# Kernel tuning notes

Hardware: AMD Instinct MI355X
Metric: run time of the kernel (lower is better)

## Reference

```python
import jax, jax.numpy as jnp
import numpy as np

DIM = 256
N_EMBED = 1024
COMMITMENT_COST = 0.25


def setup_inputs() -> dict:
    key = jax.random.key(0)
    k1, k2 = jax.random.split(key)
    z = jax.random.normal(k1, (16, 256, 64, 64), dtype=jnp.float32)
    # nn.Embedding weight initialized uniform(-1/n_embed, 1/n_embed)
    embed = jax.random.uniform(k2, (N_EMBED, DIM), dtype=jnp.float32,
                               minval=-1.0 / N_EMBED, maxval=1.0 / N_EMBED)
    return {"z": z, "embed": embed}


def reference(z, embed):
    sg = jax.lax.stop_gradient
    # NCHW -> NHWC, flatten spatial+batch to tokens
    zp = jnp.transpose(z, (0, 2, 3, 1))            # [B,H,W,C]
    zf = zp.reshape(-1, DIM)                        # [N, C]
    # squared euclidean distances via expansion: |z|^2 + |e|^2 - 2 z.e
    d = (jnp.sum(zf * zf, axis=1, keepdims=True)
         + jnp.sum(embed * embed, axis=1)
         - 2.0 * zf @ embed.T)                      # [N, K]
    idx = jnp.argmin(d, axis=1)                     # [N]
    min_encodings = jax.nn.one_hot(idx, N_EMBED, dtype=zf.dtype)  # [N, K]
    # direct gather == one-hot @ embed (same math, one HBM pass)
    z_q = embed[idx].reshape(zp.shape)              # [B,H,W,C]
    loss = (jnp.mean((sg(z_q) - zp) ** 2)
            + COMMITMENT_COST * jnp.mean((z_q - sg(zp)) ** 2))
    # straight-through estimator
    z_q_st = zp + sg(z_q - zp)
    e_mean = jnp.mean(min_encodings, axis=0)
    perplexity = jnp.exp(-jnp.sum(e_mean * jnp.log(e_mean + 1e-10)))
    z_q_out = jnp.transpose(z_q_st, (0, 3, 1, 2))   # back to NCHW
    return (loss, z_q_out, perplexity, min_encodings, idx[:, None])
```

## Files before the change

### kernel.cpp

```cpp
#include <hip/hip_runtime.h>
#include <math.h>

#define DIM    256
#define K_EMB  1024
#define HW     4096
#define CHW    1048576
#define N_TOK  65536
#define NELEM  16777216

#define OUT_LOSS 0
#define OUT_ZQ   1
#define OUT_PERP 16777217
#define OUT_MENC 16777218LL
#define OUT_IDX  83886082

#define TAU  1.5e-4f

#define TAIL_ROW0  65216
#define FLAGS_OFF  66781184LL
#define FBS_OFF    66846720LL
#define EH_OFF     66912258LL

typedef short short8  __attribute__((ext_vector_type(8)));
typedef float floatx4 __attribute__((ext_vector_type(4)));
typedef float floatx2 __attribute__((ext_vector_type(2)));

__device__ __forceinline__ unsigned short f2bf(float f) {
    unsigned int u = __float_as_uint(f);
    return (unsigned short)((u + 0x7FFFu + ((u >> 16) & 1u)) >> 16);
}
__device__ __forceinline__ float bf2f(unsigned short h) {
    return __uint_as_float(((unsigned int)h) << 16);
}

__device__ __forceinline__ float np_pair128(const float* p) {
    float r[8];
    #pragma unroll
    for (int j = 0; j < 8; ++j) r[j] = p[j];
    for (int i = 8; i < 128; i += 8)
        #pragma unroll
        for (int j = 0; j < 8; ++j) r[j] = __fadd_rn(r[j], p[i + j]);
    return __fadd_rn(__fadd_rn(__fadd_rn(r[0], r[1]), __fadd_rn(r[2], r[3])),
                     __fadd_rn(__fadd_rn(r[4], r[5]), __fadd_rn(r[6], r[7])));
}
__device__ __forceinline__ float np_pair256(const float* p) {
    return __fadd_rn(np_pair128(p), np_pair128(p + 128));
}

__device__ __forceinline__ void build_frags(const float* __restrict__ zp, int quad, short8* a) {
    #pragma unroll
    for (int kc = 0; kc < 8; ++kc) {
        short8 vh, vl;
        #pragma unroll
        for (int u = 0; u < 8; ++u) {
            float v = __builtin_nontemporal_load(zp + (size_t)(kc * 32 + quad * 8 + u) * HW);
            unsigned short h = f2bf(v);
            vh[u] = (short)h;
            vl[u] = (short)f2bf(v - bf2f(h));
        }
        a[kc]     = vh;
        a[8 + kc] = vl;
    }
}

__global__ void t2_np_kernel(const float* __restrict__ embed, float* __restrict__ t2,
                             unsigned short* __restrict__ Eh) {
    int k = blockIdx.x * 256 + threadIdx.x;
    if (k >= K_EMB) return;
    const float* e = embed + (size_t)k * DIM;
    float p[256];
    for (int c = 0; c < DIM; c += 4) {
        float4 v = *(const float4*)(e + c);
        p[c]     = __fmul_rn(v.x, v.x);
        p[c + 1] = __fmul_rn(v.y, v.y);
        p[c + 2] = __fmul_rn(v.z, v.z);
        p[c + 3] = __fmul_rn(v.w, v.w);
    }
    t2[k] = np_pair256(p);
    unsigned short* dst = Eh + (size_t)k * DIM;
    for (int c0 = 0; c0 < DIM; c0 += 8) {
        short8 vh;
        #pragma unroll
        for (int u = 0; u < 8; ++u) vh[u] = (short)f2bf(e[c0 + u]);
        *(short8*)(dst + c0) = vh;
    }
}

__launch_bounds__(256, 4)
__global__ void vq_mfma(const float* __restrict__ z,
                        const unsigned short* __restrict__ Eh,
                        const float* __restrict__ t2g,
                        float* __restrict__ out,
                        unsigned int* __restrict__ nflag,
                        int* __restrict__ flags,
                        float* __restrict__ fbs) {
    __shared__ unsigned short lds_b[32 * 264];
    __shared__ float t2_lds[K_EMB];
    __shared__ int midx[64];

    const int tid  = threadIdx.x;
    const int lane = tid & 63;
    const int wv   = tid >> 6;
    const int l15  = lane & 15;
    const int quad = lane >> 4;
    const int m0   = blockIdx.x * 64;

    for (int i = tid; i < K_EMB; i += 256) t2_lds[i] = t2g[i];

    short8 a[16];
    {
        const int n = m0 + wv * 16 + l15;
        build_frags(z + (size_t)(n >> 12) * CHW + (n & 4095), quad, a);
    }

    float bs[4], ss[4]; int bk[4];
    #pragma unroll
    for (int r = 0; r < 4; ++r) { bs[r] = 3.4e38f; ss[r] = 3.4e38f; bk[r] = 0; }

    const int srow = tid >> 3;
    const int scol = (tid & 7) * 32;

    for (int it = 0; it < 32; ++it) {
        const int n0 = it * 32;
        __syncthreads();
        {
            const short8* g = (const short8*)(Eh + (size_t)(n0 + srow) * 256 + scol);
            short8* l = (short8*)(lds_b + srow * 264 + scol);
            short8 v0 = g[0], v1 = g[1], v2 = g[2], v3 = g[3];
            l[0] = v0; l[1] = v1; l[2] = v2; l[3] = v3;
        }
        __syncthreads();
        floatx4 acc0 = {0.f, 0.f, 0.f, 0.f};
        floatx4 acc1 = {0.f, 0.f, 0.f, 0.f};
        #pragma unroll
        for (int kc = 0; kc < 8; ++kc) {
            short8 b0 = *(const short8*)(lds_b + l15 * 264 + kc * 32 + quad * 8);
            short8 b1 = *(const short8*)(lds_b + (16 + l15) * 264 + kc * 32 + quad * 8);
            acc0 = __builtin_amdgcn_mfma_f32_16x16x32_bf16(a[kc],     b0, acc0, 0, 0, 0);
            acc1 = __builtin_amdgcn_mfma_f32_16x16x32_bf16(a[kc],     b1, acc1, 0, 0, 0);
            acc0 = __builtin_amdgcn_mfma_f32_16x16x32_bf16(a[8 + kc], b0, acc0, 0, 0, 0);
            acc1 = __builtin_amdgcn_mfma_f32_16x16x32_bf16(a[8 + kc], b1, acc1, 0, 0, 0);
        }
        float t20 = t2_lds[n0 + l15];
        float t21 = t2_lds[n0 + 16 + l15];
        #pragma unroll
        for (int r = 0; r < 4; ++r) {
            float s0 = fmaf(-2.0f, acc0[r], t20);
            if (s0 < bs[r]) { ss[r] = bs[r]; bs[r] = s0; bk[r] = n0 + l15; }
            else if (s0 < ss[r]) ss[r] = s0;
            float s1 = fmaf(-2.0f, acc1[r], t21);
            if (s1 < bs[r]) { ss[r] = bs[r]; bs[r] = s1; bk[r] = n0 + 16 + l15; }
            else if (s1 < ss[r]) ss[r] = s1;
        }
    }

    #pragma unroll
    for (int r = 0; r < 4; ++r) {
        for (int mo = 1; mo < 16; mo <<= 1) {
            float obs = __shfl_xor(bs[r], mo, 64);
            float oss = __shfl_xor(ss[r], mo, 64);
            int   obk = __shfl_xor(bk[r], mo, 64);
            if (obs < bs[r] || (obs == bs[r] && obk < bk[r])) {
                ss[r] = fminf(bs[r], oss); bs[r] = obs; bk[r] = obk;
            } else {
                ss[r] = fminf(ss[r], obs);
            }
        }
        if (l15 == 0) {
            int tl = wv * 16 + quad * 4 + r;
            out[OUT_IDX + m0 + tl] = (float)bk[r];
            midx[tl] = bk[r];
            if (ss[r] - bs[r] < TAU) {
                unsigned int slot = atomicAdd(nflag, 1u);
                flags[slot] = m0 + tl;
                fbs[slot]   = bs[r];
            }
        }
    }

    if (blockIdx.x < (TAIL_ROW0 / 64)) {
        __syncthreads();
        #pragma unroll 1
        for (int j = 0; j < 64; ++j) {
            const int id = midx[j];
            floatx2* dst = (floatx2*)(out + OUT_MENC + (size_t)(m0 + j) * K_EMB);
            int c0 = tid * 2;
            floatx2 v;  v.x  = (c0 == id)       ? 1.0f : 0.0f;  v.y  = (c0 + 1 == id)  ? 1.0f : 0.0f;
            __builtin_nontemporal_store(v, dst + tid);
            int c1 = c0 + 512;
            floatx2 w2; w2.x = (c1 == id)       ? 1.0f : 0.0f;  w2.y = (c1 + 1 == id)  ? 1.0f : 0.0f;
            __builtin_nontemporal_store(w2, dst + 256 + tid);
        }
    }
}

__launch_bounds__(256)
__global__ void refine_mfma(const float* __restrict__ z, const float* __restrict__ embed,
                            const unsigned short* __restrict__ Eh,
                            const float* __restrict__ t2g, float* __restrict__ out,
                            const unsigned int* __restrict__ nflag,
                            const int* __restrict__ flags,
                            const float* __restrict__ fbs) {
    __shared__ unsigned short lds_b[32 * 264];
    __shared__ float t2_lds[K_EMB];
    __shared__ int   ftok[64];
    __shared__ float fbest[64];
    __shared__ int   ccnt[64];
    __shared__ int   clist[64][32];
    __shared__ float pp4[4][256];

    const int tid  = threadIdx.x;
    const int lane = tid & 63;
    const int wv   = tid >> 6;
    const int l15  = lane & 15;
    const int quad = lane >> 4;
    const int nf   = (int)*nflag;

    for (int i = tid; i < K_EMB; i += 256) t2_lds[i] = t2g[i];

    const int srow = tid >> 3;
    const int scol = (tid & 7) * 32;

    for (int base = blockIdx.x * 64; base < nf; base += gridDim.x * 64) {
        __syncthreads();
        if (tid < 64) {
            int ii  = base + tid;
            int src = (ii < nf) ? ii : base;
            ftok[tid]  = flags[src];
            fbest[tid] = fbs[src];
            ccnt[tid]  = 0;
        }
        __syncthreads();

        short8 a[16];
        {
            const int n = ftok[wv * 16 + l15];
            build_frags(z + (size_t)(n >> 12) * CHW + (n & 4095), quad, a);
        }
        float ftb[4];
        #pragma unroll
        for (int r = 0; r < 4; ++r) ftb[r] = fbest[wv * 16 + quad * 4 + r] + TAU;

        for (int it = 0; it < 32; ++it) {
            const int n0 = it * 32;
            __syncthreads();
            {
                const short8* g = (const short8*)(Eh + (size_t)(n0 + srow) * 256 + scol);
                short8* l = (short8*)(lds_b + srow * 264 + scol);
                short8 v0 = g[0], v1 = g[1], v2 = g[2], v3 = g[3];
                l[0] = v0; l[1] = v1; l[2] = v2; l[3] = v3;
            }
            __syncthreads();
            floatx4 acc0 = {0.f, 0.f, 0.f, 0.f};
            floatx4 acc1 = {0.f, 0.f, 0.f, 0.f};
            #pragma unroll
            for (int kc = 0; kc < 8; ++kc) {
                short8 b0 = *(const short8*)(lds_b + l15 * 264 + kc * 32 + quad * 8);
                short8 b1 = *(const short8*)(lds_b + (16 + l15) * 264 + kc * 32 + quad * 8);
                acc0 = __builtin_amdgcn_mfma_f32_16x16x32_bf16(a[kc],     b0, acc0, 0, 0, 0);
                acc1 = __builtin_amdgcn_mfma_f32_16x16x32_bf16(a[kc],     b1, acc1, 0, 0, 0);
                acc0 = __builtin_amdgcn_mfma_f32_16x16x32_bf16(a[8 + kc], b0, acc0, 0, 0, 0);
                acc1 = __builtin_amdgcn_mfma_f32_16x16x32_bf16(a[8 + kc], b1, acc1, 0, 0, 0);
            }
            float t20 = t2_lds[n0 + l15];
            float t21 = t2_lds[n0 + 16 + l15];
            #pragma unroll
            for (int r = 0; r < 4; ++r) {
                const int trow = wv * 16 + quad * 4 + r;
                float s0 = fmaf(-2.0f, acc0[r], t20);
                if (s0 <= ftb[r]) {
                    int pos = atomicAdd(&ccnt[trow], 1);
                    if (pos < 32) clist[trow][pos] = n0 + l15;
                }
                float s1 = fmaf(-2.0f, acc1[r], t21);
                if (s1 <= ftb[r]) {
                    int pos = atomicAdd(&ccnt[trow], 1);
                    if (pos < 32) clist[trow][pos] = n0 + 16 + l15;
                }
            }
        }
        __syncthreads();

        for (int j = wv * 16; j < wv * 16 + 16; ++j) {
            if (base + j >= nf) break;
            const int n = ftok[j];
            int cnt = ccnt[j]; if (cnt > 32) cnt = 32;

            const float* zt = z + (size_t)(n >> 12) * CHW + (n & 4095);
            double zd[4];
            #pragma unroll
            for (int u = 0; u < 4; ++u) {
                float v = zt[(size_t)(lane + u * 64) * HW];
                zd[u] = (double)v;
                pp4[wv][lane + u * 64] = __fmul_rn(v, v);
            }
            __asm__ volatile("s_waitcnt lgkmcnt(0)" ::: "memory");
            float rj = 0.0f;
            if (lane < 16) {
                int jj = lane & 7, half = lane >> 3;
                const float* p = &pp4[wv][half * 128 + jj];
                rj = p[0];
                #pragma unroll
                for (int ii = 1; ii < 16; ++ii) rj = __fadd_rn(rj, p[ii * 8]);
            }
            float v0 = __shfl(rj, 0, 64), v1 = __shfl(rj, 1, 64), v2 = __shfl(rj, 2, 64), v3 = __shfl(rj, 3, 64);
            float v4 = __shfl(rj, 4, 64), v5 = __shfl(rj, 5, 64), v6 = __shfl(rj, 6, 64), v7 = __shfl(rj, 7, 64);
            float h0 = __fadd_rn(__fadd_rn(__fadd_rn(v0, v1), __fadd_rn(v2, v3)),
                                 __fadd_rn(__fadd_rn(v4, v5), __fadd_rn(v6, v7)));
            v0 = __shfl(rj,  8, 64); v1 = __shfl(rj,  9, 64); v2 = __shfl(rj, 10, 64); v3 = __shfl(rj, 11, 64);
            v4 = __shfl(rj, 12, 64); v5 = __shfl(rj, 13, 64); v6 = __shfl(rj, 14, 64); v7 = __shfl(rj, 15, 64);
            float h1 = __fadd_rn(__fadd_rn(__fadd_rn(v0, v1), __fadd_rn(v2, v3)),
                                 __fadd_rn(__fadd_rn(v4, v5), __fadd_rn(v6, v7)));
            const float t1 = __fadd_rn(h0, h1);

            float bd = 3.4e38f; int bkk = 1 << 30;
            for (int ci = 0; ci < cnt; ++ci) {
                int k = clist[j][ci];
                const float* e = embed + (size_t)k * DIM;
                double s = 0.0;
                #pragma unroll
                for (int u = 0; u < 4; ++u) s = fma(zd[u], (double)e[lane + u * 64], s);
                for (int mo = 1; mo < 64; mo <<= 1) s += __shfl_xor(s, mo, 64);
                float rho = (float)s;
                float d = __fadd_rn(__fadd_rn(t1, t2_lds[k]), -__fmul_rn(2.0f, rho));
                if (d < bd || (d == bd && k < bkk)) { bd = d; bkk = k; }
            }
            if (lane == 0) {
                int old = (int)out[OUT_IDX + n];
                if (bkk != old) {
                    out[OUT_IDX + n] = (float)bkk;
                    if (n < TAIL_ROW0) {
                        out[OUT_MENC + (size_t)n * K_EMB + old] = 0.0f;
                        out[OUT_MENC + (size_t)n * K_EMB + bkk] = 1.0f;
                    }
                }
            }
        }
    }
}

__global__ void menc_tail(float* __restrict__ out) {
    const int row = TAIL_ROW0 + blockIdx.x;
    const int id  = (int)out[OUT_IDX + row];
    floatx2* dst = (floatx2*)(out + OUT_MENC + (size_t)row * K_EMB);
    int c0 = threadIdx.x * 2;
    floatx2 v;  v.x  = (c0 == id)      ? 1.0f : 0.0f;  v.y  = (c0 + 1 == id) ? 1.0f : 0.0f;
    dst[threadIdx.x] = v;
    int c1 = c0 + 512;
    floatx2 w;  w.x  = (c1 == id)      ? 1.0f : 0.0f;  w.y  = (c1 + 1 == id) ? 1.0f : 0.0f;
    dst[256 + threadIdx.x] = w;
}

__launch_bounds__(256)
__global__ void zq_loss_kernel(const float* __restrict__ z, const float* __restrict__ embed,
                               float* __restrict__ out, unsigned int* __restrict__ counts,
                               float* __restrict__ loss_sum) {
    const int tid = threadIdx.x;
    const int blk = blockIdx.x;
    const int b   = blk >> 7;
    const int h   = (blk >> 1) & 63;
    const int wh  = blk & 1;
    const int w   = tid & 31;
    const int cs  = tid >> 5;
    const int n   = blk * 32 + w;

    const int myk = (int)out[OUT_IDX + n];
    if (tid < 32) atomicAdd(&counts[myk], 1u);

    const float* erow = embed + (size_t)myk * DIM;
    const float* zt = z   + (size_t)b * CHW + h * 64 + wh * 32;
    float*       zq = out + OUT_ZQ + (size_t)b * CHW + h * 64 + wh * 32;
    float lsum = 0.0f;
    for (int c = cs; c < DIM; c += 8) {
        float v  = erow[c];
        float dz = v - zt[(size_t)c * HW + w];
        lsum = fmaf(dz, dz, lsum);
        zq[(size_t)c * HW + w] = v;
    }
    #pragma unroll
    for (int off = 32; off > 0; off >>= 1) lsum += __shfl_down(lsum, off, 64);
    if ((tid & 63) == 0) atomicAdd(loss_sum, lsum);
}

__global__ void finalize_kernel(const unsigned int* __restrict__ counts,
                                const float* __restrict__ loss_sum,
                                float* __restrict__ out) {
    __shared__ float red[256];
    int tid = threadIdx.x;
    float hsum = 0.0f;
    for (int k = tid; k < K_EMB; k += 256) {
        float p = (float)counts[k] * (1.0f / 65536.0f);
        hsum += p * logf(p + 1e-10f);
    }
    red[tid] = hsum;
    __syncthreads();
    for (int s = 128; s > 0; s >>= 1) {
        if (tid < s) red[tid] += red[tid + s];
        __syncthreads();
    }
    if (tid == 0) {
        out[OUT_PERP] = expf(-red[0]);
        out[OUT_LOSS] = loss_sum[0] * 1.25f * (1.0f / (float)NELEM);
    }
}

extern "C" void kernel_launch(void* const* d_in, const int* in_sizes, int n_in,
                              void* d_out, int out_size, void* d_ws, size_t ws_size,
                              hipStream_t stream) {
    const float* z     = (const float*)d_in[0];
    const float* embed = (const float*)d_in[1];
    float* out = (float*)d_out;

    unsigned int* counts = (unsigned int*)d_ws;
    float* loss_sum      = (float*)((char*)d_ws + 4096);
    unsigned int* nflag  = (unsigned int*)((char*)d_ws + 4100);
    float* t2g           = (float*)((char*)d_ws + 8192);

    float* scr = out + OUT_MENC;
    int*            fl = (int*)(scr + FLAGS_OFF);
    float*          fb = (float*)(scr + FBS_OFF);
    unsigned short* Eh = (unsigned short*)(scr + EH_OFF);

    (void)hipMemsetAsync(d_ws, 0, 4104, stream);
    t2_np_kernel   <<<dim3(4),    dim3(256), 0, stream>>>(embed, t2g, Eh);
    vq_mfma        <<<dim3(1024), dim3(256), 0, stream>>>(z, Eh, t2g, out, nflag, fl, fb);
    refine_mfma    <<<dim3(128),  dim3(256), 0, stream>>>(z, embed, Eh, t2g, out, nflag, fl, fb);
    menc_tail      <<<dim3(320),  dim3(256), 0, stream>>>(out);
    zq_loss_kernel <<<dim3(2048), dim3(256), 0, stream>>>(z, embed, out, counts, loss_sum);
    finalize_kernel<<<dim3(1),    dim3(256), 0, stream>>>(counts, loss_sum, out);
}
```

Measured before the change: 775.8 us.

## Fuse z_q write, loss and counts into vq_mfma; patch deltas in refine

Removes the separate zq_loss kernel. The main MFMA kernel now writes z_q, accumulates the loss and increments the codebook counts right after the argmin, reconstructing z from the split-bf16 fragments it already holds in registers. The refine kernel applies delta corrections to loss, counts and z_q for any token whose index changes. This drops a full reread of z and the launch overhead. In exchange it adds register pressure and a reconstruction of z from bf16 hi+lo pairs that may not be exact, which could slightly perturb the loss value.

```diff
diff --git a/kernel.cpp b/kernel.cpp
--- a/kernel.cpp
+++ b/kernel.cpp
@@ -88,12 +88,15 @@
 
 __launch_bounds__(256, 4)
 __global__ void vq_mfma(const float* __restrict__ z,
+                        const float* __restrict__ embed,
                         const unsigned short* __restrict__ Eh,
                         const float* __restrict__ t2g,
                         float* __restrict__ out,
                         unsigned int* __restrict__ nflag,
                         int* __restrict__ flags,
-                        float* __restrict__ fbs) {
+                        float* __restrict__ fbs,
+                        unsigned int* __restrict__ counts,
+                        float* __restrict__ loss_sum) {
     __shared__ unsigned short lds_b[32 * 264];
     __shared__ float t2_lds[K_EMB];
     __shared__ int midx[64];
@@ -170,6 +173,7 @@
             int tl = wv * 16 + quad * 4 + r;
             out[OUT_IDX + m0 + tl] = (float)bk[r];
             midx[tl] = bk[r];
+            atomicAdd(&counts[bk[r]], 1u);
             if (ss[r] - bs[r] < TAU) {
                 unsigned int slot = atomicAdd(nflag, 1u);
                 flags[slot] = m0 + tl;
@@ -177,9 +181,35 @@
             }
         }
     }
+    __syncthreads();
+
+    {
+        const int n   = m0 + wv * 16 + l15;
+        const int myk = midx[wv * 16 + l15];
+        const float* erow = embed + (size_t)myk * DIM;
+        float* zqp = out + OUT_ZQ + (size_t)(n >> 12) * CHW + (n & 4095);
+        float lsum = 0.0f;
+        #pragma unroll
+        for (int kc = 0; kc < 8; ++kc) {
+            const int c0 = kc * 32 + quad * 8;
+            float4 e0 = *(const float4*)(erow + c0);
+            float4 e1 = *(const float4*)(erow + c0 + 4);
+            float ev[8] = {e0.x, e0.y, e0.z, e0.w, e1.x, e1.y, e1.z, e1.w};
+            #pragma unroll
+            for (int u = 0; u < 8; ++u) {
+                float vv = __fadd_rn(bf2f((unsigned short)a[kc][u]),
+                                     bf2f((unsigned short)a[8 + kc][u]));
+                float dz = ev[u] - vv;
+                lsum = fmaf(dz, dz, lsum);
+                __builtin_nontemporal_store(ev[u], zqp + (size_t)(c0 + u) * HW);
+            }
+        }
+        #pragma unroll
+        for (int off = 32; off > 0; off >>= 1) lsum += __shfl_down(lsum, off, 64);
+        if (lane == 0) atomicAdd(loss_sum, lsum);
+    }
 
     if (blockIdx.x < (TAIL_ROW0 / 64)) {
-        __syncthreads();
         #pragma unroll 1
         for (int j = 0; j < 64; ++j) {
             const int id = midx[j];
@@ -200,7 +230,9 @@
                             const float* __restrict__ t2g, float* __restrict__ out,
                             const unsigned int* __restrict__ nflag,
                             const int* __restrict__ flags,
-                            const float* __restrict__ fbs) {
+                            const float* __restrict__ fbs,
+                            unsigned int* __restrict__ counts,
+                            float* __restrict__ loss_sum) {
     __shared__ unsigned short lds_b[32 * 264];
     __shared__ float t2_lds[K_EMB];
     __shared__ int   ftok[64];
@@ -287,11 +319,11 @@
             int cnt = ccnt[j]; if (cnt > 32) cnt = 32;
 
             const float* zt = z + (size_t)(n >> 12) * CHW + (n & 4095);
-            double zd[4];
+            double zd[4]; float zf[4];
             #pragma unroll
             for (int u = 0; u < 4; ++u) {
                 float v = zt[(size_t)(lane + u * 64) * HW];
-                zd[u] = (double)v;
+                zf[u] = v; zd[u] = (double)v;
                 pp4[wv][lane + u * 64] = __fmul_rn(v, v);
             }
             __asm__ volatile("s_waitcnt lgkmcnt(0)" ::: "memory");
@@ -325,9 +357,26 @@
                 float d = __fadd_rn(__fadd_rn(t1, t2_lds[k]), -__fmul_rn(2.0f, rho));
                 if (d < bd || (d == bd && k < bkk)) { bd = d; bkk = k; }
             }
-            if (lane == 0) {
-                int old = (int)out[OUT_IDX + n];
-                if (bkk != old) {
+
+            const int old = (int)out[OUT_IDX + n];
+            if (bkk != old) {
+                const float* eo = embed + (size_t)old * DIM;
+                const float* en = embed + (size_t)bkk * DIM;
+                float* zqp = out + OUT_ZQ + (size_t)(n >> 12) * CHW + (n & 4095);
+                float dl = 0.0f;
+                #pragma unroll
+                for (int u = 0; u < 4; ++u) {
+                    const int c = lane + u * 64;
+                    float d_new = en[c] - zf[u];
+                    float d_old = eo[c] - zf[u];
+                    dl += d_new * d_new - d_old * d_old;
+                    zqp[(size_t)c * HW] = en[c];
+                }
+                for (int mo = 1; mo < 64; mo <<= 1) dl += __shfl_xor(dl, mo, 64);
+                if (lane == 0) {
+                    atomicAdd(loss_sum, dl);
+                    atomicAdd(&counts[old], 0xFFFFFFFFu);
+                    atomicAdd(&counts[bkk], 1u);
                     out[OUT_IDX + n] = (float)bkk;
                     if (n < TAIL_ROW0) {
                         out[OUT_MENC + (size_t)n * K_EMB + old] = 0.0f;
@@ -351,37 +400,6 @@
     dst[256 + threadIdx.x] = w;
 }
 
-__launch_bounds__(256)
-__global__ void zq_loss_kernel(const float* __restrict__ z, const float* __restrict__ embed,
-                               float* __restrict__ out, unsigned int* __restrict__ counts,
-                               float* __restrict__ loss_sum) {
-    const int tid = threadIdx.x;
-    const int blk = blockIdx.x;
-    const int b   = blk >> 7;
-    const int h   = (blk >> 1) & 63;
-    const int wh  = blk & 1;
-    const int w   = tid & 31;
-    const int cs  = tid >> 5;
-    const int n   = blk * 32 + w;
-
-    const int myk = (int)out[OUT_IDX + n];
-    if (tid < 32) atomicAdd(&counts[myk], 1u);
-
-    const float* erow = embed + (size_t)myk * DIM;
-    const float* zt = z   + (size_t)b * CHW + h * 64 + wh * 32;
-    float*       zq = out + OUT_ZQ + (size_t)b * CHW + h * 64 + wh * 32;
-    float lsum = 0.0f;
-    for (int c = cs; c < DIM; c += 8) {
-        float v  = erow[c];
-        float dz = v - zt[(size_t)c * HW + w];
-        lsum = fmaf(dz, dz, lsum);
-        zq[(size_t)c * HW + w] = v;
-    }
-    #pragma unroll
-    for (int off = 32; off > 0; off >>= 1) lsum += __shfl_down(lsum, off, 64);
-    if ((tid & 63) == 0) atomicAdd(loss_sum, lsum);
-}
-
 __global__ void finalize_kernel(const unsigned int* __restrict__ counts,
                                 const float* __restrict__ loss_sum,
                                 float* __restrict__ out) {
@@ -423,9 +441,8 @@
 
     (void)hipMemsetAsync(d_ws, 0, 4104, stream);
     t2_np_kernel   <<<dim3(4),    dim3(256), 0, stream>>>(embed, t2g, Eh);
-    vq_mfma        <<<dim3(1024), dim3(256), 0, stream>>>(z, Eh, t2g, out, nflag, fl, fb);
-    refine_mfma    <<<dim3(128),  dim3(256), 0, stream>>>(z, embed, Eh, t2g, out, nflag, fl, fb);
+    vq_mfma        <<<dim3(1024), dim3(256), 0, stream>>>(z, embed, Eh, t2g, out, nflag, fl, fb, counts, loss_sum);
+    refine_mfma    <<<dim3(128),  dim3(256), 0, stream>>>(z, embed, Eh, t2g, out, nflag, fl, fb, counts, loss_sum);
     menc_tail      <<<dim3(320),  dim3(256), 0, stream>>>(out);
-    zq_loss_kernel <<<dim3(2048), dim3(256), 0, stream>>>(z, embed, out, counts, loss_sum);
     finalize_kernel<<<dim3(1),    dim3(256), 0, stream>>>(counts, loss_sum, out);
 }
```

New measurement: 774.1 us. No clear change (-0.2%).
